# Performance work log

Measured on AMD Instinct MI355X. Metric: run time of the kernel, lower is better.

Reference implementation:

```python
import jax, jax.numpy as jnp
import numpy as np
import math

B, S, D = 4, 2048, 1024
N_HEADS = 16
D_FF = 4096
T_DIM = 256
KEEP_RATIO = 0.7
EPS = 1e-5


def _layernorm(x):
    mu = jnp.mean(x, axis=-1, keepdims=True)
    var = jnp.mean((x - mu) ** 2, axis=-1, keepdims=True)
    return (x - mu) * jax.lax.rsqrt(var + EPS)


def _ada_ln(x, cond, W, b):
    # cond: (B, T_DIM); W: (2D, T_DIM)
    p = jax.nn.silu(cond) @ W.T + b            # (B, 2D)
    gamma, beta = jnp.split(p, 2, axis=-1)
    return _layernorm(x) * (1.0 + gamma[:, None, :]) + beta[:, None, :]


def _mha(h, in_w, in_b, out_w, out_b):
    b, s, d = h.shape
    hd = d // N_HEADS
    qkv = h @ in_w.T + in_b                     # (b, s, 3d)
    q, k, v = jnp.split(qkv, 3, axis=-1)
    def heads(t):
        return t.reshape(b, s, N_HEADS, hd).transpose(0, 2, 1, 3)
    q, k, v = heads(q), heads(k), heads(v)
    scores = jnp.einsum('bhqd,bhkd->bhqk', q, k) / math.sqrt(hd)
    attn = jax.nn.softmax(scores, axis=-1)
    o = jnp.einsum('bhqk,bhkd->bhqd', attn, v)  # (b, h, s, hd)
    o = o.transpose(0, 2, 1, 3).reshape(b, s, d)
    return o @ out_w.T + out_b


def setup_inputs() -> dict:
    key = jax.random.key(0)
    ks = jax.random.split(key, 24)
    sc = 0.02
    return {
        'x': jax.random.normal(ks[0], (B, S, D), jnp.float32),
        't_emb': jax.random.normal(ks[1], (B, T_DIM), jnp.float32),
        'tr_w1': jax.random.normal(ks[2], (32, D), jnp.float32) * sc,
        'tr_b1': jnp.zeros((32,), jnp.float32),
        'tr_w2': jax.random.normal(ks[3], (1, 32), jnp.float32) * sc,
        'tr_b2': jnp.zeros((1,), jnp.float32),
        'ln1_w': jax.random.normal(ks[4], (2 * D, T_DIM), jnp.float32) * sc,
        'ln1_b': jnp.zeros((2 * D,), jnp.float32),
        'ln2_w': jax.random.normal(ks[5], (2 * D, T_DIM), jnp.float32) * sc,
        'ln2_b': jnp.zeros((2 * D,), jnp.float32),
        'in_proj_w': jax.random.normal(ks[6], (3 * D, D), jnp.float32) * sc,
        'in_proj_b': jnp.zeros((3 * D,), jnp.float32),
        'out_w': jax.random.normal(ks[7], (D, D), jnp.float32) * sc,
        'out_b': jnp.zeros((D,), jnp.float32),
        'ffn_w1': jax.random.normal(ks[8], (D_FF, D), jnp.float32) * sc,
        'ffn_b1': jnp.zeros((D_FF,), jnp.float32),
        'ffn_w2': jax.random.normal(ks[9], (D, D_FF), jnp.float32) * sc,
        'ffn_b2': jnp.zeros((D,), jnp.float32),
        # torch inits gates to zero; use small randn so the block is non-trivial
        'gate_attn': jax.random.normal(ks[10], (1, 1, D), jnp.float32) * sc,
        'gate_ffn': jax.random.normal(ks[11], (1, 1, D), jnp.float32) * sc,
    }


def reference(x, t_emb, tr_w1, tr_b1, tr_w2, tr_b2, ln1_w, ln1_b, ln2_w, ln2_b,
              in_proj_w, in_proj_b, out_w, out_b, ffn_w1, ffn_b1, ffn_w2, ffn_b2,
              gate_attn, gate_ffn):
    b, s, d = x.shape
    num_keep = max(int(s * KEEP_RATIO), 1)

    # token importance on detached x (stop_gradient mirrors x.detach())
    xd = jax.lax.stop_gradient(x)
    imp = jax.nn.silu(xd @ tr_w1.T + tr_b1) @ tr_w2.T + tr_b2  # (b, s, 1)
    imp = imp[..., 0]
    _, idx = jax.lax.top_k(imp, num_keep)
    idx = jnp.sort(idx, axis=-1)                               # (b, num_keep)

    x_sel = jnp.take_along_axis(x, idx[..., None], axis=1)     # (b, k, d)

    h = _ada_ln(x_sel, t_emb, ln1_w, ln1_b)
    h = _mha(h, in_proj_w, in_proj_b, out_w, out_b)
    x_sel = x_sel + gate_attn * h

    h = _ada_ln(x_sel, t_emb, ln2_w, ln2_b)
    h = jax.nn.gelu(h @ ffn_w1.T + ffn_b1, approximate=False) @ ffn_w2.T + ffn_b2
    x_sel = x_sel + gate_ffn * h

    batch_idx = jnp.arange(b)[:, None]
    return x.at[batch_idx, idx].set(x_sel)
```

## Files before the change

kernel.cpp:

```cpp
#include <hip/hip_runtime.h>
#include <hip/hip_bf16.h>
#include <cmath>
#include <cstdint>

typedef __bf16 bf16;
typedef __bf16 bf16x8 __attribute__((ext_vector_type(8)));
typedef __bf16 bf16x4 __attribute__((ext_vector_type(4)));
typedef float  f32x4  __attribute__((ext_vector_type(4)));

constexpr int B_   = 4;
constexpr int S_   = 2048;
constexpr int D_   = 1024;
constexpr int H_   = 16;
constexpr int DFF_ = 4096;
constexpr int TD_  = 256;
constexpr int KEEP = 1433;
constexpr int M_TOT = B_ * KEEP;
constexpr int MPAD  = 5888;
constexpr int QT64  = (KEEP + 63) / 64;
constexpr int NKV   = (KEEP + 63) / 64;
constexpr float EPS = 1e-5f;
constexpr float QSCALE = 0.18033688011112042f;

__device__ __forceinline__ f32x4 mfma16(bf16x8 a, bf16x8 b, f32x4 c) {
  return __builtin_amdgcn_mfma_f32_16x16x32_bf16(a, b, c, 0, 0, 0);
}

#define GLOAD_LDS(gp, lp)                                                     \
  __builtin_amdgcn_global_load_lds(                                           \
      (const __attribute__((address_space(1))) void*)(gp),                    \
      (__attribute__((address_space(3))) void*)(lp), 16, 0, 0)

__global__ __launch_bounds__(256) void k_importance(
    const float* __restrict__ x, const float* __restrict__ w1,
    const float* __restrict__ b1, const float* __restrict__ w2,
    const float* __restrict__ b2, double* __restrict__ imp)
{
  const int lane = threadIdx.x & 63, w = threadIdx.x >> 6;
  const int tok0 = blockIdx.x * 16 + w * 4;
  const float* xb = x + (size_t)tok0 * D_ + lane * 4;
  double r[4] = {};
  for (int u0 = 0; u0 < 32; u0 += 8) {
    const float* wb = w1 + (size_t)u0 * D_ + lane * 4;
    double acc[4][8] = {};
#pragma unroll 2
    for (int c = 0; c < D_; c += 256) {
      float4 xv[4], wv[8];
#pragma unroll
      for (int i = 0; i < 4; ++i)
        xv[i] = *(const float4*)(xb + (size_t)i * D_ + c);
#pragma unroll
      for (int u = 0; u < 8; ++u)
        wv[u] = *(const float4*)(wb + (size_t)u * D_ + c);
#pragma unroll
      for (int i = 0; i < 4; ++i)
#pragma unroll
        for (int u = 0; u < 8; ++u) {
          acc[i][u] += (double)xv[i].x * (double)wv[u].x;
          acc[i][u] += (double)xv[i].y * (double)wv[u].y;
          acc[i][u] += (double)xv[i].z * (double)wv[u].z;
          acc[i][u] += (double)xv[i].w * (double)wv[u].w;
        }
    }
#pragma unroll
    for (int i = 0; i < 4; ++i)
#pragma unroll
      for (int u = 0; u < 8; ++u) {
        double s = acc[i][u];
        for (int o = 32; o > 0; o >>= 1) s += __shfl_xor(s, o);
        const double h = s + (double)b1[u0 + u];
        const double sv = h / (1.0 + exp(-h));
        r[i] += sv * (double)w2[u0 + u];
      }
  }
  if (lane == 0) {
#pragma unroll
    for (int i = 0; i < 4; ++i)
      imp[tok0 + i] = r[i] + (double)b2[0];
  }
}

__global__ __launch_bounds__(256) void k_rank(const double* __restrict__ imp,
                                              int* __restrict__ rank)
{
  const int b = blockIdx.x >> 5;
  const int seg = blockIdx.x & 31;
  __shared__ double vals[S_];
  const double* ib = imp + (size_t)b * S_;
  for (int i = threadIdx.x; i < S_ / 2; i += 256)
    ((double2*)vals)[i] = ((const double2*)ib)[i];
  __syncthreads();
  const int tl = threadIdx.x >> 2;
  const int part = threadIdx.x & 3;
  const int s = seg * 64 + tl;
  const double v = vals[s];
  int cnt = 0;
  for (int j = part * 512; j < (part + 1) * 512; ++j) {
    double u = vals[j];
    cnt += (u > v) || (u == v && j < s);
  }
  cnt += __shfl_xor(cnt, 1);
  cnt += __shfl_xor(cnt, 2);
  if (part == 0) rank[b * S_ + s] = cnt;
}

__global__ __launch_bounds__(256) void k_compact(const int* __restrict__ rank,
                                                 int* __restrict__ idx)
{
  const int b = blockIdx.x;
  __shared__ int wcnt[4];
  __shared__ int base_s;
  if (threadIdx.x == 0) base_s = 0;
  __syncthreads();
  const int t = threadIdx.x, lane = t & 63, w = t >> 6;
  for (int c = 0; c < S_ / 256; ++c) {
    const int s = c * 256 + t;
    const bool kept = rank[b * S_ + s] < KEEP;
    unsigned long long m = __ballot(kept);
    int piw = __popcll(m & ((1ull << lane) - 1ull));
    if (lane == 0) wcnt[w] = __popcll(m);
    __syncthreads();
    int off = base_s;
    for (int i = 0; i < w; ++i) off += wcnt[i];
    if (kept) idx[b * KEEP + off + piw] = s;
    __syncthreads();
    if (t == 0) base_s += wcnt[0] + wcnt[1] + wcnt[2] + wcnt[3];
    __syncthreads();
  }
}

__global__ __launch_bounds__(256) void k_condproj(
    const float* __restrict__ temb,
    const float* __restrict__ W1, const float* __restrict__ b1f,
    float* __restrict__ p1,
    const float* __restrict__ W2, const float* __restrict__ b2f,
    float* __restrict__ p2)
{
  int gw = (int)((blockIdx.x * 256 + threadIdx.x) >> 6);
  const int lane = threadIdx.x & 63;
  const float* W = W1; const float* bias = b1f; float* p = p1;
  if (gw >= 8192) { gw -= 8192; W = W2; bias = b2f; p = p2; }
  const int b = gw >> 11;
  const int row = gw & 2047;
  const float* te = temb + (size_t)b * TD_;
  const float* wr = W + (size_t)row * TD_;
  float acc = 0.f;
  for (int i = lane; i < TD_; i += 64) {
    float c = te[i];
    acc += (c / (1.f + __expf(-c))) * wr[i];
  }
  for (int o = 32; o > 0; o >>= 1) acc += __shfl_down(acc, o);
  if (lane == 0) p[(size_t)b * 2 * D_ + row] = acc + bias[row];
}

__global__ void k_f2b(const float* __restrict__ s0, const float* __restrict__ s1,
                      const float* __restrict__ s2, const float* __restrict__ s3,
                      bf16* __restrict__ d0, bf16* __restrict__ d1,
                      bf16* __restrict__ d2, bf16* __restrict__ d3)
{
  const int g = blockIdx.x * 256 + threadIdx.x;
  const float* src; bf16* dst; int off;
  if (g < 786432)       { src = s0; dst = d0; off = g; }
  else if (g < 1048576) { src = s1; dst = d1; off = g - 786432; }
  else if (g < 2097152) { src = s2; dst = d2; off = g - 1048576; }
  else                  { src = s3; dst = d3; off = g - 2097152; }
  float4 v = ((const float4*)src)[off];
  bf16x4 o = {(bf16)v.x, (bf16)v.y, (bf16)v.z, (bf16)v.w};
  ((bf16x4*)dst)[off] = o;
}

__global__ __launch_bounds__(256) void k_adaln(
    const float* __restrict__ xsrc, const int* __restrict__ idx,
    const float* __restrict__ p, bf16* __restrict__ hout)
{
  const int r = blockIdx.x, t = threadIdx.x;
  bf16* orow = hout + (size_t)r * D_;
  if (r >= M_TOT) {
    bf16x4 z = {(bf16)0.f, (bf16)0.f, (bf16)0.f, (bf16)0.f};
    ((bf16x4*)orow)[t] = z;
    return;
  }
  const int b = r / KEEP, j = r - b * KEEP;
  const int s = idx[b * KEEP + j];
  const float* xr = xsrc + ((size_t)(b * S_ + s)) * D_;
  float4 v = ((const float4*)xr)[t];
  __shared__ float red[8];
  float sum = v.x + v.y + v.z + v.w;
  for (int o = 32; o > 0; o >>= 1) sum += __shfl_down(sum, o);
  const int lane = t & 63, w = t >> 6;
  if (lane == 0) red[w] = sum;
  __syncthreads();
  const float mu = (red[0] + red[1] + red[2] + red[3]) * (1.f / D_);
  const float dx = v.x - mu, dy = v.y - mu, dz = v.z - mu, dw = v.w - mu;
  float vs = dx * dx + dy * dy + dz * dz + dw * dw;
  for (int o = 32; o > 0; o >>= 1) vs += __shfl_down(vs, o);
  if (lane == 0) red[4 + w] = vs;
  __syncthreads();
  const float rstd = rsqrtf((red[4] + red[5] + red[6] + red[7]) * (1.f / D_) + EPS);
  const float* gp = p + (size_t)b * 2 * D_;
  float4 g  = ((const float4*)gp)[t];
  float4 be = ((const float4*)(gp + D_))[t];
  bf16x4 o;
  o[0] = (bf16)(dx * rstd * (1.f + g.x) + be.x);
  o[1] = (bf16)(dy * rstd * (1.f + g.y) + be.y);
  o[2] = (bf16)(dz * rstd * (1.f + g.z) + be.z);
  o[3] = (bf16)(dw * rstd * (1.f + g.w) + be.w);
  ((bf16x4*)orow)[t] = o;
}

template <int BN, int MODE>
__global__ __launch_bounds__(256) void k_gemm(
    const bf16* __restrict__ A, const bf16* __restrict__ W,
    const float* __restrict__ bias, bf16* __restrict__ Cbf,
    const float* __restrict__ gate, const int* __restrict__ idx,
    float* __restrict__ resid, int N, int K, int gn)
{
  constexpr int WN = BN / 2;
  constexpr int NJ = WN / 16;
  constexpr int WIT = BN / 32;
  __shared__ bf16 As[2][128 * 64];
  __shared__ bf16 Ws[2][BN * 64];
  const int t = threadIdx.x, lane = t & 63;
  const int w = t >> 6, wr = w >> 1, wc = w & 1;
  const int fr = lane & 15, fq = lane >> 4;

  const int nwg = gridDim.x, orig = blockIdx.x;
  const int q8 = nwg >> 3, r8 = nwg & 7;
  const int xc = orig & 7, pos = orig >> 3;
  const int wgid = (xc < r8 ? xc * (q8 + 1) : r8 * (q8 + 1) + (xc - r8) * q8) + pos;
  const int bm = wgid / gn, bn = wgid - bm * gn;

  const bf16* Ab = A + (size_t)bm * 128 * K;
  const bf16* Wb = W + (size_t)bn * BN * K;

  const bf16* pA[4];
  const bf16* pW[WIT];
#pragma unroll
  for (int it = 0; it < 4; ++it) {
    const int e = it * 256 + t;
    const int row = e >> 3, pc = e & 7;
    const int lc = pc ^ (row & 7);
    pA[it] = Ab + (size_t)row * K + lc * 8;
  }
#pragma unroll
  for (int it = 0; it < WIT; ++it) {
    const int e = it * 256 + t;
    const int row = e >> 3, pc = e & 7;
    const int lc = pc ^ (row & 7);
    pW[it] = Wb + (size_t)row * K + lc * 8;
  }

  auto stage = [&](int buf) {
#pragma unroll
    for (int it = 0; it < 4; ++it) {
      GLOAD_LDS(pA[it], &As[buf][0] + (it * 256 + t) * 8);
      pA[it] += 64;
    }
#pragma unroll
    for (int it = 0; it < WIT; ++it) {
      GLOAD_LDS(pW[it], &Ws[buf][0] + (it * 256 + t) * 8);
      pW[it] += 64;
    }
  };

  f32x4 acc[4][NJ] = {};
  stage(0);
  const int nkt = K >> 6;
  int cur = 0;
  for (int kt = 0; kt < nkt; ++kt) {
    __syncthreads();
    if (kt + 1 < nkt) stage(cur ^ 1);
    const char* Al = (const char*)&As[cur][0];
    const char* Wl = (const char*)&Ws[cur][0];
#pragma unroll
    for (int kk = 0; kk < 2; ++kk) {
      bf16x8 af[4], wf[NJ];
#pragma unroll
      for (int i = 0; i < 4; ++i)
        af[i] = *(const bf16x8*)(Al + (wr * 64 + i * 16 + fr) * 128 +
                                 (((kk * 4 + fq) ^ (fr & 7)) << 4));
#pragma unroll
      for (int j = 0; j < NJ; ++j)
        wf[j] = *(const bf16x8*)(Wl + (wc * WN + j * 16 + fr) * 128 +
                                 (((kk * 4 + fq) ^ (fr & 7)) << 4));
#pragma unroll
      for (int i = 0; i < 4; ++i)
#pragma unroll
        for (int j = 0; j < NJ; ++j)
          acc[i][j] = mfma16(af[i], wf[j], acc[i][j]);
    }
    cur ^= 1;
  }

  if (MODE == 2) {
#pragma unroll
    for (int i = 0; i < 4; ++i) {
#pragma unroll
      for (int r = 0; r < 4; ++r) {
        const int m = bm * 128 + wr * 64 + i * 16 + fq * 4 + r;
        if (m < M_TOT) {
          const int b = m / KEEP, jj = m - b * KEEP;
          const int s = idx[b * KEEP + jj];
          float* rp = resid + ((size_t)(b * S_ + s)) * D_ + bn * BN + wc * WN + fr;
          const float* gp = gate + bn * BN + wc * WN + fr;
          const float* bp = bias + bn * BN + wc * WN + fr;
#pragma unroll
          for (int j = 0; j < NJ; ++j)
            rp[j * 16] += gp[j * 16] * (acc[i][j][r] + bp[j * 16]);
        }
      }
    }
  } else {
#pragma unroll
    for (int i = 0; i < 4; ++i) {
#pragma unroll
      for (int j = 0; j < NJ; ++j) {
#pragma unroll
        for (int r = 0; r < 4; ++r) {
          const int m = bm * 128 + wr * 64 + i * 16 + fq * 4 + r;
          const int n = bn * BN + wc * WN + j * 16 + fr;
          float v = acc[i][j][r] + bias[n];
          if (MODE == 0) {
            if (n < D_) v *= QSCALE;
            Cbf[(size_t)m * N + n] = (bf16)v;
          } else {
            float gl = 0.5f * v * (1.f + erff(v * 0.70710678118654752f));
            Cbf[(size_t)m * N + n] = (bf16)gl;
          }
        }
      }
    }
  }
}

__global__ __launch_bounds__(256) void k_attn(const bf16* __restrict__ qkv,
                                              bf16* __restrict__ out)
{
  __shared__ bf16 Klds[2][64 * 64];
  __shared__ bf16 Vlds[2][64 * 64];

  const int t = threadIdx.x;
  const int lane = t & 63, w = t >> 6;
  const int fr = lane & 15, fq = lane >> 4;

  const int orig = blockIdx.x;
  const int wgid = (orig & 7) * 184 + (orig >> 3);
  const int qt = wgid % QT64;
  const int hb = wgid / QT64;
  const int h = hb & 15, b = hb >> 4;

  const size_t rowbase = (size_t)b * KEEP;
  const size_t RS = 3 * D_;
  const bf16* kbase = qkv + rowbase * RS + D_ + h * 64;
  const bf16* vbase = qkv + rowbase * RS + 2 * D_ + h * 64;

  const int wq0 = qt * 64 + w * 16;
  const int qrow = min(wq0 + fr, KEEP - 1);
  const bf16* qp = qkv + (rowbase + qrow) * RS + h * 64 + fq * 8;
  const bf16x8 qf0 = *(const bf16x8*)qp;
  const bf16x8 qf1 = *(const bf16x8*)(qp + 32);

  f32x4 o[4] = {};
  float mrow = -INFINITY, lrow = 0.f;

  const int p0 = t, p1 = 256 + t;
  auto kaddr = [&](int p, int kv) {
    const int row = p >> 3, c8p = p & 7;
    const int c8 = c8p ^ ((row & 7) ^ (row >> 3));
    const int gr = min(kv + row, KEEP - 1);
    return kbase + (size_t)gr * RS + c8 * 8;
  };
  auto vaddr = [&](int p, int kv) {
    const int db = p >> 7, ksub = (p >> 3) & 15, jr = (p >> 1) & 3,
              c8lo = p & 1;
    const int vrow = ksub * 4 + jr, vc8 = db * 2 + c8lo;
    const int gr = min(kv + vrow, KEEP - 1);
    return vbase + (size_t)gr * RS + vc8 * 8;
  };
  const bf16* kp0 = kaddr(p0, 0);
  const bf16* kp1 = kaddr(p1, 0);
  const bf16* vp0 = vaddr(p0, 0);
  const bf16* vp1 = vaddr(p1, 0);

  auto stage_fast = [&](int buf) {
    GLOAD_LDS(kp0, &Klds[buf][0] + p0 * 8);
    GLOAD_LDS(kp1, &Klds[buf][0] + p1 * 8);
    GLOAD_LDS(vp0, &Vlds[buf][0] + p0 * 8);
    GLOAD_LDS(vp1, &Vlds[buf][0] + p1 * 8);
    kp0 += 64 * RS; kp1 += 64 * RS; vp0 += 64 * RS; vp1 += 64 * RS;
  };
  auto stage_last = [&](int buf, int kv) {
    GLOAD_LDS(kaddr(p0, kv), &Klds[buf][0] + p0 * 8);
    GLOAD_LDS(kaddr(p1, kv), &Klds[buf][0] + p1 * 8);
    GLOAD_LDS(vaddr(p0, kv), &Vlds[buf][0] + p0 * 8);
    GLOAD_LDS(vaddr(p1, kv), &Vlds[buf][0] + p1 * 8);
  };

  stage_fast(0);
  int cur = 0;

  const unsigned vbase_lds0 =
      (unsigned)(size_t)(__attribute__((address_space(3))) bf16*)&Vlds[0][0];
  const unsigned vbase_lds1 =
      (unsigned)(size_t)(__attribute__((address_space(3))) bf16*)&Vlds[1][0];

  for (int ti = 0; ti < NKV; ++ti) {
    const int kv = ti * 64;
    __syncthreads();
    if (ti < NKV - 2) stage_fast(cur ^ 1);
    else if (ti == NKV - 2) stage_last(cur ^ 1, kv + 64);

    const char* Kl = (const char*)&Klds[cur][0];

    f32x4 sc[4];
    __builtin_amdgcn_s_setprio(1);
#pragma unroll
    for (int f = 0; f < 4; ++f) {
      const int row = ((f >> 1) << 5) + ((fr >> 2) << 3) + ((f & 1) << 1) +
                      (fr & 1) + (((fr >> 1) & 1) << 2);
      const int swz = (row & 7) ^ (row >> 3);
      const bf16x8 kf0 = *(const bf16x8*)(Kl + row * 128 + ((fq ^ swz) << 4));
      const bf16x8 kf1 =
          *(const bf16x8*)(Kl + row * 128 + (((fq ^ 4) ^ swz) << 4));
      f32x4 s = {0.f, 0.f, 0.f, 0.f};
      s = mfma16(kf0, qf0, s);
      s = mfma16(kf1, qf1, s);
      sc[f] = s;
    }
    __builtin_amdgcn_s_setprio(0);

    const unsigned vb =
        (cur ? vbase_lds1 : vbase_lds0) + ((unsigned)fq << 7);
    bf16x4 v0[8], v1[8];
    asm volatile(
        "ds_read_b64_tr_b16 %0, %8 offset:0\n\t"
        "ds_read_b64_tr_b16 %1, %8 offset:128\n\t"
        "ds_read_b64_tr_b16 %2, %8 offset:2048\n\t"
        "ds_read_b64_tr_b16 %3, %8 offset:2176\n\t"
        "ds_read_b64_tr_b16 %4, %8 offset:4096\n\t"
        "ds_read_b64_tr_b16 %5, %8 offset:4224\n\t"
        "ds_read_b64_tr_b16 %6, %8 offset:6144\n\t"
        "ds_read_b64_tr_b16 %7, %8 offset:6272"
        : "=&v"(v0[0]), "=&v"(v0[1]), "=&v"(v0[2]), "=&v"(v0[3]),
          "=&v"(v0[4]), "=&v"(v0[5]), "=&v"(v0[6]), "=&v"(v0[7])
        : "v"(vb));
    asm volatile(
        "ds_read_b64_tr_b16 %0, %8 offset:1024\n\t"
        "ds_read_b64_tr_b16 %1, %8 offset:1152\n\t"
        "ds_read_b64_tr_b16 %2, %8 offset:3072\n\t"
        "ds_read_b64_tr_b16 %3, %8 offset:3200\n\t"
        "ds_read_b64_tr_b16 %4, %8 offset:5120\n\t"
        "ds_read_b64_tr_b16 %5, %8 offset:5248\n\t"
        "ds_read_b64_tr_b16 %6, %8 offset:7168\n\t"
        "ds_read_b64_tr_b16 %7, %8 offset:7296"
        : "=&v"(v1[0]), "=&v"(v1[1]), "=&v"(v1[2]), "=&v"(v1[3]),
          "=&v"(v1[4]), "=&v"(v1[5]), "=&v"(v1[6]), "=&v"(v1[7])
        : "v"(vb));

    if (ti == NKV - 1) {
#pragma unroll
      for (int f = 0; f < 4; ++f)
#pragma unroll
        for (int r = 0; r < 4; ++r) {
          const int kl = ((f >> 1) << 5) + (fq << 3) + ((f & 1) << 1) +
                         (r & 1) + ((r >> 1) << 2);
          if (kv + kl >= KEEP) sc[f][r] = -INFINITY;
        }
    }
    float m0 = fmaxf(fmaxf(sc[0][0], sc[0][1]), sc[0][2]);
    float m1 = fmaxf(fmaxf(sc[0][3], sc[1][0]), sc[1][1]);
    float m2 = fmaxf(fmaxf(sc[1][2], sc[1][3]), sc[2][0]);
    float m3 = fmaxf(fmaxf(sc[2][1], sc[2][2]), sc[2][3]);
    float m4 = fmaxf(fmaxf(sc[3][0], sc[3][1]), sc[3][2]);
    float mx = fmaxf(fmaxf(m0, m1), m2);
    mx = fmaxf(fmaxf(mx, m3), fmaxf(m4, sc[3][3]));
    mx = fmaxf(mx, __shfl_xor(mx, 16));
    mx = fmaxf(mx, __shfl_xor(mx, 32));

    const bool noresc = __all(mx <= mrow + 8.f);
    const float mnew = noresc ? mrow : fmaxf(mrow, mx);
    float ps = 0.f;
    bf16 pe[4][4];
#pragma unroll
    for (int f = 0; f < 4; ++f)
#pragma unroll
      for (int r = 0; r < 4; ++r) {
        const float pv = exp2f(sc[f][r] - mnew);
        ps += pv;
        pe[f][r] = (bf16)pv;
      }
    ps += __shfl_xor(ps, 16);
    ps += __shfl_xor(ps, 32);
    if (!noresc) {
      const float fac = exp2f(mrow - mnew);
      lrow *= fac;
#pragma unroll
      for (int db = 0; db < 4; ++db) {
        o[db][0] *= fac; o[db][1] *= fac; o[db][2] *= fac; o[db][3] *= fac;
      }
      mrow = mnew;
    }
    lrow += ps;

    const bf16x8 pb[2] = {
        {pe[0][0], pe[0][1], pe[1][0], pe[1][1],
         pe[0][2], pe[0][3], pe[1][2], pe[1][3]},
        {pe[2][0], pe[2][1], pe[3][0], pe[3][1],
         pe[2][2], pe[2][3], pe[3][2], pe[3][3]}};

    asm volatile("s_waitcnt lgkmcnt(0)" ::: "memory");
    __builtin_amdgcn_sched_barrier(0);

    const bf16x8 vf00 = __builtin_shufflevector(v0[0], v0[1], 0,1,2,3,4,5,6,7);
    const bf16x8 vf01 = __builtin_shufflevector(v0[2], v0[3], 0,1,2,3,4,5,6,7);
    const bf16x8 vf02 = __builtin_shufflevector(v0[4], v0[5], 0,1,2,3,4,5,6,7);
    const bf16x8 vf03 = __builtin_shufflevector(v0[6], v0[7], 0,1,2,3,4,5,6,7);
    const bf16x8 vf10 = __builtin_shufflevector(v1[0], v1[1], 0,1,2,3,4,5,6,7);
    const bf16x8 vf11 = __builtin_shufflevector(v1[2], v1[3], 0,1,2,3,4,5,6,7);
    const bf16x8 vf12 = __builtin_shufflevector(v1[4], v1[5], 0,1,2,3,4,5,6,7);
    const bf16x8 vf13 = __builtin_shufflevector(v1[6], v1[7], 0,1,2,3,4,5,6,7);
    __builtin_amdgcn_s_setprio(1);
    o[0] = mfma16(vf00, pb[0], o[0]);
    o[1] = mfma16(vf01, pb[0], o[1]);
    o[2] = mfma16(vf02, pb[0], o[2]);
    o[3] = mfma16(vf03, pb[0], o[3]);
    o[0] = mfma16(vf10, pb[1], o[0]);
    o[1] = mfma16(vf11, pb[1], o[1]);
    o[2] = mfma16(vf12, pb[1], o[2]);
    o[3] = mfma16(vf13, pb[1], o[3]);
    __builtin_amdgcn_s_setprio(0);
    cur ^= 1;
  }

  const int q = wq0 + fr;
  if (q < KEEP) {
    const float inv = 1.f / lrow;
#pragma unroll
    for (int db = 0; db < 4; ++db) {
      bf16x4 wv = {(bf16)(o[db][0] * inv), (bf16)(o[db][1] * inv),
                   (bf16)(o[db][2] * inv), (bf16)(o[db][3] * inv)};
      *(bf16x4*)(out + (rowbase + q) * (size_t)D_ + h * 64 + db * 16 + fq * 4) =
          wv;
    }
  }
}

extern "C" void kernel_launch(void* const* d_in, const int* in_sizes, int n_in,
                              void* d_out, int out_size, void* d_ws, size_t ws_size,
                              hipStream_t stream)
{
  (void)in_sizes; (void)n_in; (void)out_size; (void)ws_size;
  const float* x      = (const float*)d_in[0];
  const float* t_emb  = (const float*)d_in[1];
  const float* tr_w1  = (const float*)d_in[2];
  const float* tr_b1  = (const float*)d_in[3];
  const float* tr_w2  = (const float*)d_in[4];
  const float* tr_b2  = (const float*)d_in[5];
  const float* ln1_w  = (const float*)d_in[6];
  const float* ln1_b  = (const float*)d_in[7];
  const float* ln2_w  = (const float*)d_in[8];
  const float* ln2_b  = (const float*)d_in[9];
  const float* in_w   = (const float*)d_in[10];
  const float* in_b   = (const float*)d_in[11];
  const float* out_w  = (const float*)d_in[12];
  const float* out_b  = (const float*)d_in[13];
  const float* f1_w   = (const float*)d_in[14];
  const float* f1_b   = (const float*)d_in[15];
  const float* f2_w   = (const float*)d_in[16];
  const float* f2_b   = (const float*)d_in[17];
  const float* gate_a = (const float*)d_in[18];
  const float* gate_f = (const float*)d_in[19];

  char* ws = (char*)d_ws;
  size_t off = 0;
  auto alloc = [&](size_t bytes) -> char* {
    char* p = ws + off;
    off = (off + bytes + 255) & ~(size_t)255;
    return p;
  };
  double* imp  = (double*)alloc((size_t)B_ * S_ * 8);
  int* rank    = (int*)alloc((size_t)B_ * S_ * 4);
  int* idx     = (int*)alloc((size_t)B_ * KEEP * 4);
  float* p1    = (float*)alloc((size_t)B_ * 2 * D_ * 4);
  float* p2    = (float*)alloc((size_t)B_ * 2 * D_ * 4);
  bf16* w_in   = (bf16*)alloc((size_t)3 * D_ * D_ * 2);
  bf16* w_out  = (bf16*)alloc((size_t)D_ * D_ * 2);
  bf16* w_f1   = (bf16*)alloc((size_t)DFF_ * D_ * 2);
  bf16* w_f2   = (bf16*)alloc((size_t)D_ * DFF_ * 2);
  bf16* h_bf   = (bf16*)alloc((size_t)MPAD * D_ * 2);
  bf16* big    = (bf16*)alloc((size_t)MPAD * (3 * D_ + D_) * 2);
  bf16* qkv    = big;
  bf16* attn   = big + (size_t)MPAD * 3 * D_;
  bf16* ffn1   = big;

  hipMemcpyAsync(d_out, x, (size_t)B_ * S_ * D_ * 4, hipMemcpyDeviceToDevice, stream);

  k_importance<<<B_ * S_ / 16, 256, 0, stream>>>(x, tr_w1, tr_b1, tr_w2, tr_b2, imp);
  k_rank<<<B_ * 32, 256, 0, stream>>>(imp, rank);
  k_compact<<<B_, 256, 0, stream>>>(rank, idx);

  k_condproj<<<4096, 256, 0, stream>>>(t_emb, ln1_w, ln1_b, p1, ln2_w, ln2_b, p2);
  k_f2b<<<12288, 256, 0, stream>>>(in_w, out_w, f1_w, f2_w, w_in, w_out, w_f1, w_f2);

  k_adaln<<<MPAD, 256, 0, stream>>>(x, idx, p1, h_bf);
  k_gemm<128, 0><<<46 * 24, 256, 0, stream>>>(
      h_bf, w_in, in_b, qkv, nullptr, nullptr, nullptr, 3 * D_, D_, 24);
  k_attn<<<QT64 * H_ * B_, 256, 0, stream>>>(qkv, attn);
  k_gemm<64, 2><<<46 * 16, 256, 0, stream>>>(
      attn, w_out, out_b, nullptr, gate_a, idx, (float*)d_out, D_, D_, 16);
  k_adaln<<<MPAD, 256, 0, stream>>>((const float*)d_out, idx, p2, h_bf);
  k_gemm<128, 1><<<46 * 32, 256, 0, stream>>>(
      h_bf, w_f1, f1_b, ffn1, nullptr, nullptr, nullptr, DFF_, D_, 32);
  k_gemm<64, 2><<<46 * 16, 256, 0, stream>>>(
      ffn1, w_f2, f2_b, nullptr, gate_f, idx, (float*)d_out, D_, DFF_, 16);
}
```

Measured before the change: 448.5 us.

## Fuse prep kernels into one launch and shrink GEMM K-tile to 32

Merges token-importance scoring, weight fp32-to-bf16 conversion, the output copy of x and the AdaLN condition projections into a single block-partitioned prep kernel, replacing the separate memcpy and three launches. It also halves the GEMM K tile from 64 to 32 with a matching 4-chunk swizzle, reducing LDS footprint per block. The fusion removes launch overhead and lets the independent work overlap. The smaller K tile doubles barrier and stage iterations per GEMM, which may reduce MFMA density.

```diff
diff --git a/kernel.cpp b/kernel.cpp
--- a/kernel.cpp
+++ b/kernel.cpp
@@ -31,52 +31,94 @@
       (const __attribute__((address_space(1))) void*)(gp),                    \
       (__attribute__((address_space(3))) void*)(lp), 16, 0, 0)
 
-__global__ __launch_bounds__(256) void k_importance(
-    const float* __restrict__ x, const float* __restrict__ w1,
-    const float* __restrict__ b1, const float* __restrict__ w2,
-    const float* __restrict__ b2, double* __restrict__ imp)
+__global__ __launch_bounds__(256) void k_prep(
+    const float* __restrict__ x, const float* __restrict__ tr_w1,
+    const float* __restrict__ tr_b1, const float* __restrict__ tr_w2,
+    const float* __restrict__ tr_b2, double* __restrict__ imp,
+    const float* __restrict__ in_w, const float* __restrict__ out_w,
+    const float* __restrict__ f1_w, const float* __restrict__ f2_w,
+    bf16* __restrict__ w_in, bf16* __restrict__ w_out,
+    bf16* __restrict__ w_f1, bf16* __restrict__ w_f2,
+    float* __restrict__ dout,
+    const float* __restrict__ temb,
+    const float* __restrict__ ln1_w, const float* __restrict__ ln1_b,
+    float* __restrict__ p1,
+    const float* __restrict__ ln2_w, const float* __restrict__ ln2_b,
+    float* __restrict__ p2)
 {
-  const int lane = threadIdx.x & 63, w = threadIdx.x >> 6;
-  const int tok0 = blockIdx.x * 16 + w * 4;
-  const float* xb = x + (size_t)tok0 * D_ + lane * 4;
-  double r[4] = {};
-  for (int u0 = 0; u0 < 32; u0 += 8) {
-    const float* wb = w1 + (size_t)u0 * D_ + lane * 4;
-    double acc[4][8] = {};
+  const int bid = blockIdx.x;
+  if (bid < 512) {
+    const int lane = threadIdx.x & 63, w = threadIdx.x >> 6;
+    const int tok0 = bid * 16 + w * 4;
+    const float* xb = x + (size_t)tok0 * D_ + lane * 4;
+    double r[4] = {};
+    for (int u0 = 0; u0 < 32; u0 += 8) {
+      const float* wb = tr_w1 + (size_t)u0 * D_ + lane * 4;
+      double acc[4][8] = {};
 #pragma unroll 2
-    for (int c = 0; c < D_; c += 256) {
-      float4 xv[4], wv[8];
+      for (int c = 0; c < D_; c += 256) {
+        float4 xv[4], wv[8];
+#pragma unroll
+        for (int i = 0; i < 4; ++i)
+          xv[i] = *(const float4*)(xb + (size_t)i * D_ + c);
+#pragma unroll
+        for (int u = 0; u < 8; ++u)
+          wv[u] = *(const float4*)(wb + (size_t)u * D_ + c);
+#pragma unroll
+        for (int i = 0; i < 4; ++i)
+#pragma unroll
+          for (int u = 0; u < 8; ++u) {
+            acc[i][u] += (double)xv[i].x * (double)wv[u].x;
+            acc[i][u] += (double)xv[i].y * (double)wv[u].y;
+            acc[i][u] += (double)xv[i].z * (double)wv[u].z;
+            acc[i][u] += (double)xv[i].w * (double)wv[u].w;
+          }
+      }
 #pragma unroll
       for (int i = 0; i < 4; ++i)
-        xv[i] = *(const float4*)(xb + (size_t)i * D_ + c);
-#pragma unroll
-      for (int u = 0; u < 8; ++u)
-        wv[u] = *(const float4*)(wb + (size_t)u * D_ + c);
+#pragma unroll
+        for (int u = 0; u < 8; ++u) {
+          double s = acc[i][u];
+          for (int o = 32; o > 0; o >>= 1) s += __shfl_xor(s, o);
+          const double h = s + (double)tr_b1[u0 + u];
+          const double sv = h / (1.0 + exp(-h));
+          r[i] += sv * (double)tr_w2[u0 + u];
+        }
+    }
+    if (lane == 0) {
 #pragma unroll
       for (int i = 0; i < 4; ++i)
-#pragma unroll
-        for (int u = 0; u < 8; ++u) {
-          acc[i][u] += (double)xv[i].x * (double)wv[u].x;
-          acc[i][u] += (double)xv[i].y * (double)wv[u].y;
-          acc[i][u] += (double)xv[i].z * (double)wv[u].z;
-          acc[i][u] += (double)xv[i].w * (double)wv[u].w;
-        }
-    }
-#pragma unroll
-    for (int i = 0; i < 4; ++i)
-#pragma unroll
-      for (int u = 0; u < 8; ++u) {
-        double s = acc[i][u];
-        for (int o = 32; o > 0; o >>= 1) s += __shfl_xor(s, o);
-        const double h = s + (double)b1[u0 + u];
-        const double sv = h / (1.0 + exp(-h));
-        r[i] += sv * (double)w2[u0 + u];
-      }
-  }
-  if (lane == 0) {
-#pragma unroll
-    for (int i = 0; i < 4; ++i)
-      imp[tok0 + i] = r[i] + (double)b2[0];
+        imp[tok0 + i] = r[i] + (double)tr_b2[0];
+    }
+  } else if (bid < 12800) {
+    const int g = (bid - 512) * 256 + threadIdx.x;
+    const float* src; bf16* dst; int off;
+    if (g < 786432)       { src = in_w;  dst = w_in;  off = g; }
+    else if (g < 1048576) { src = out_w; dst = w_out; off = g - 786432; }
+    else if (g < 2097152) { src = f1_w;  dst = w_f1;  off = g - 1048576; }
+    else                  { src = f2_w;  dst = w_f2;  off = g - 2097152; }
+    float4 v = ((const float4*)src)[off];
+    bf16x4 o = {(bf16)v.x, (bf16)v.y, (bf16)v.z, (bf16)v.w};
+    ((bf16x4*)dst)[off] = o;
+  } else if (bid < 20992) {
+    const int g = (bid - 12800) * 256 + threadIdx.x;
+    ((float4*)dout)[g] = ((const float4*)x)[g];
+  } else {
+    int gw = (int)(((bid - 20992) * 256 + threadIdx.x) >> 6);
+    const int lane = threadIdx.x & 63;
+    const float* W = ln1_w; const float* bias = ln1_b; float* p = p1;
+    if (gw >= 8192) { gw -= 8192; W = ln2_w; bias = ln2_b; p = p2; }
+    const int b = gw >> 11;
+    const int row = gw & 2047;
+    const float* te = temb + (size_t)b * TD_;
+    const float* wr = W + (size_t)row * TD_;
+    float acc = 0.f;
+    for (int i = lane; i < TD_; i += 64) {
+      float c = te[i];
+      acc += (c / (1.f + __expf(-c))) * wr[i];
+    }
+    for (int o = 32; o > 0; o >>= 1) acc += __shfl_down(acc, o);
+    if (lane == 0) p[(size_t)b * 2 * D_ + row] = acc + bias[row];
   }
 }
 
@@ -127,46 +169,6 @@
     if (t == 0) base_s += wcnt[0] + wcnt[1] + wcnt[2] + wcnt[3];
     __syncthreads();
   }
-}
-
-__global__ __launch_bounds__(256) void k_condproj(
-    const float* __restrict__ temb,
-    const float* __restrict__ W1, const float* __restrict__ b1f,
-    float* __restrict__ p1,
-    const float* __restrict__ W2, const float* __restrict__ b2f,
-    float* __restrict__ p2)
-{
-  int gw = (int)((blockIdx.x * 256 + threadIdx.x) >> 6);
-  const int lane = threadIdx.x & 63;
-  const float* W = W1; const float* bias = b1f; float* p = p1;
-  if (gw >= 8192) { gw -= 8192; W = W2; bias = b2f; p = p2; }
-  const int b = gw >> 11;
-  const int row = gw & 2047;
-  const float* te = temb + (size_t)b * TD_;
-  const float* wr = W + (size_t)row * TD_;
-  float acc = 0.f;
-  for (int i = lane; i < TD_; i += 64) {
-    float c = te[i];
-    acc += (c / (1.f + __expf(-c))) * wr[i];
-  }
-  for (int o = 32; o > 0; o >>= 1) acc += __shfl_down(acc, o);
-  if (lane == 0) p[(size_t)b * 2 * D_ + row] = acc + bias[row];
-}
-
-__global__ void k_f2b(const float* __restrict__ s0, const float* __restrict__ s1,
-                      const float* __restrict__ s2, const float* __restrict__ s3,
-                      bf16* __restrict__ d0, bf16* __restrict__ d1,
-                      bf16* __restrict__ d2, bf16* __restrict__ d3)
-{
-  const int g = blockIdx.x * 256 + threadIdx.x;
-  const float* src; bf16* dst; int off;
-  if (g < 786432)       { src = s0; dst = d0; off = g; }
-  else if (g < 1048576) { src = s1; dst = d1; off = g - 786432; }
-  else if (g < 2097152) { src = s2; dst = d2; off = g - 1048576; }
-  else                  { src = s3; dst = d3; off = g - 2097152; }
-  float4 v = ((const float4*)src)[off];
-  bf16x4 o = {(bf16)v.x, (bf16)v.y, (bf16)v.z, (bf16)v.w};
-  ((bf16x4*)dst)[off] = o;
 }
 
 __global__ __launch_bounds__(256) void k_adaln(
@@ -217,9 +219,9 @@
 {
   constexpr int WN = BN / 2;
   constexpr int NJ = WN / 16;
-  constexpr int WIT = BN / 32;
-  __shared__ bf16 As[2][128 * 64];
-  __shared__ bf16 Ws[2][BN * 64];
+  constexpr int WIT = BN / 64;
+  __shared__ bf16 As[2][128 * 32];
+  __shared__ bf16 Ws[2][BN * 32];
   const int t = threadIdx.x, lane = t & 63;
   const int w = t >> 6, wr = w >> 1, wc = w & 1;
   const int fr = lane & 15, fq = lane >> 4;
@@ -233,62 +235,58 @@
   const bf16* Ab = A + (size_t)bm * 128 * K;
   const bf16* Wb = W + (size_t)bn * BN * K;
 
-  const bf16* pA[4];
+  const bf16* pA[2];
   const bf16* pW[WIT];
 #pragma unroll
-  for (int it = 0; it < 4; ++it) {
+  for (int it = 0; it < 2; ++it) {
     const int e = it * 256 + t;
-    const int row = e >> 3, pc = e & 7;
-    const int lc = pc ^ (row & 7);
+    const int row = e >> 2, pc = e & 3;
+    const int lc = pc ^ (row & 3);
     pA[it] = Ab + (size_t)row * K + lc * 8;
   }
 #pragma unroll
   for (int it = 0; it < WIT; ++it) {
     const int e = it * 256 + t;
-    const int row = e >> 3, pc = e & 7;
-    const int lc = pc ^ (row & 7);
+    const int row = e >> 2, pc = e & 3;
+    const int lc = pc ^ (row & 3);
     pW[it] = Wb + (size_t)row * K + lc * 8;
   }
 
   auto stage = [&](int buf) {
 #pragma unroll
-    for (int it = 0; it < 4; ++it) {
+    for (int it = 0; it < 2; ++it) {
       GLOAD_LDS(pA[it], &As[buf][0] + (it * 256 + t) * 8);
-      pA[it] += 64;
+      pA[it] += 32;
     }
 #pragma unroll
     for (int it = 0; it < WIT; ++it) {
       GLOAD_LDS(pW[it], &Ws[buf][0] + (it * 256 + t) * 8);
-      pW[it] += 64;
+      pW[it] += 32;
     }
   };
 
   f32x4 acc[4][NJ] = {};
   stage(0);
-  const int nkt = K >> 6;
+  const int nkt = K >> 5;
   int cur = 0;
+  const int swz = ((fq ^ (fr & 3)) << 4);
   for (int kt = 0; kt < nkt; ++kt) {
     __syncthreads();
     if (kt + 1 < nkt) stage(cur ^ 1);
     const char* Al = (const char*)&As[cur][0];
     const char* Wl = (const char*)&Ws[cur][0];
-#pragma unroll
-    for (int kk = 0; kk < 2; ++kk) {
-      bf16x8 af[4], wf[NJ];
-#pragma unroll
-      for (int i = 0; i < 4; ++i)
-        af[i] = *(const bf16x8*)(Al + (wr * 64 + i * 16 + fr) * 128 +
-                                 (((kk * 4 + fq) ^ (fr & 7)) << 4));
+    bf16x8 af[4], wf[NJ];
+#pragma unroll
+    for (int i = 0; i < 4; ++i)
+      af[i] = *(const bf16x8*)(Al + (wr * 64 + i * 16 + fr) * 64 + swz);
+#pragma unroll
+    for (int j = 0; j < NJ; ++j)
+      wf[j] = *(const bf16x8*)(Wl + (wc * WN + j * 16 + fr) * 64 + swz);
+#pragma unroll
+    for (int i = 0; i < 4; ++i)
 #pragma unroll
       for (int j = 0; j < NJ; ++j)
-        wf[j] = *(const bf16x8*)(Wl + (wc * WN + j * 16 + fr) * 128 +
-                                 (((kk * 4 + fq) ^ (fr & 7)) << 4));
-#pragma unroll
-      for (int i = 0; i < 4; ++i)
-#pragma unroll
-        for (int j = 0; j < NJ; ++j)
-          acc[i][j] = mfma16(af[i], wf[j], acc[i][j]);
-    }
+        acc[i][j] = mfma16(af[i], wf[j], acc[i][j]);
     cur ^= 1;
   }
 
@@ -593,14 +591,13 @@
   bf16* attn   = big + (size_t)MPAD * 3 * D_;
   bf16* ffn1   = big;
 
-  hipMemcpyAsync(d_out, x, (size_t)B_ * S_ * D_ * 4, hipMemcpyDeviceToDevice, stream);
-
-  k_importance<<<B_ * S_ / 16, 256, 0, stream>>>(x, tr_w1, tr_b1, tr_w2, tr_b2, imp);
+  k_prep<<<25088, 256, 0, stream>>>(
+      x, tr_w1, tr_b1, tr_w2, tr_b2, imp,
+      in_w, out_w, f1_w, f2_w, w_in, w_out, w_f1, w_f2,
+      (float*)d_out,
+      t_emb, ln1_w, ln1_b, p1, ln2_w, ln2_b, p2);
   k_rank<<<B_ * 32, 256, 0, stream>>>(imp, rank);
   k_compact<<<B_, 256, 0, stream>>>(rank, idx);
-
-  k_condproj<<<4096, 256, 0, stream>>>(t_emb, ln1_w, ln1_b, p1, ln2_w, ln2_b, p2);
-  k_f2b<<<12288, 256, 0, stream>>>(in_w, out_w, f1_w, f2_w, w_in, w_out, w_f1, w_f2);
 
   k_adaln<<<MPAD, 256, 0, stream>>>(x, idx, p1, h_bf);
   k_gemm<128, 0><<<46 * 24, 256, 0, stream>>>(
```

New measurement: 462.2 us. +3.1%, slower.
